# Kernel optimization log

Hardware: AMD Instinct MI355X
Metric: run time of the kernel (lower is better)

Reference implementation:

```python
import jax, jax.numpy as jnp
import numpy as np

B, T, H, N = 4, 512, 32, 64
D = H * N  # n_embd = 2048


def setup_inputs() -> dict:
    key = jax.random.key(0)
    ks = jax.random.split(key, 8)
    f = lambda kk: jax.random.normal(kk, (B, T, H, N), dtype=jnp.float32)
    r = f(ks[0])
    w = f(ks[1])
    k = f(ks[2])
    v = f(ks[3])
    iclr = f(ks[4])
    # int8-style quantized output projection: int values in [-128,127] + per-row scale
    w_out_q = jax.random.randint(ks[5], (D, D), -128, 128, dtype=jnp.int32)
    w_out_scale = jax.random.uniform(ks[6], (D,), dtype=jnp.float32) * 0.01
    return {"r": r, "w": w, "k": k, "v": v, "iclr": iclr,
            "w_out_q": w_out_q, "w_out_scale": w_out_scale}


def _wkv7(r, w, k, v, iclr):
    """RWKV x070 WKV scan. All inputs [B,T,H,N]; returns [B,T,H*N]."""
    decay = jnp.exp(-jnp.exp(w))  # per-channel decay in (0,1), x070 parameterization
    # kk = l2-normalized key direction; a = -kk (removal), b = kk * sigmoid(iclr) (write)
    kk = k * jax.lax.rsqrt(jnp.sum(k * k, axis=-1, keepdims=True) + 1e-12)
    a = -kk
    b = kk * jax.nn.sigmoid(iclr)

    def step(state, inp):
        # state: [B,H,N,N]; each inp element: [B,H,N]
        r_t, d_t, k_t, v_t, a_t, b_t = inp
        sa = jnp.einsum('bhij,bhj->bhi', state, a_t)
        state = (state * d_t[:, :, None, :]
                 + sa[..., None] * b_t[:, :, None, :]
                 + v_t[..., None] * k_t[:, :, None, :])
        y_t = jnp.einsum('bhij,bhj->bhi', state, r_t)
        return state, y_t

    tb = lambda x: jnp.swapaxes(x, 0, 1)  # [B,T,H,N] -> [T,B,H,N]
    state0 = jnp.zeros((B, H, N, N), dtype=r.dtype)
    _, y = jax.lax.scan(step, state0, (tb(r), tb(decay), tb(k), tb(v), tb(a), tb(b)))
    return jnp.swapaxes(y, 0, 1).reshape(B, T, H * N)


def reference(r, w, k, v, iclr, w_out_q, w_out_scale):
    y = _wkv7(r, w, k, v, iclr)               # [B,T,D]
    # inline dequant of quantized output projection (per-output-row scale)
    W = w_out_q.astype(jnp.float32) * w_out_scale[:, None]  # [D,D]
    return jnp.einsum('btd,od->bto', y, W)    # [B,T,D]
```

## Files before the change

### kernel.cpp

```cpp
#include <hip/hip_runtime.h>
#include <hip/hip_bf16.h>
#include <stdint.h>

#define B_ 4
#define T_ 512
#define H_ 32
#define N_ 64
#define D_ 2048
#define M_ (B_*T_)

typedef __attribute__((ext_vector_type(4))) float f32x4;
typedef __attribute__((ext_vector_type(8))) short short8;

template <int CTRL>
__device__ __forceinline__ float dpp_add(float x) {
    int t = __builtin_amdgcn_mov_dpp(__float_as_int(x), CTRL, 0xF, 0xF, true);
    return x + __int_as_float(t);
}
__device__ __forceinline__ float bfly16(float x) {
    x = dpp_add<0xB1>(x);
    x = dpp_add<0x4E>(x);
    x = dpp_add<0x141>(x);
    x = dpp_add<0x140>(x);
    return x;
}

__device__ __forceinline__ void gld16(const float* g, float* l) {
    __builtin_amdgcn_global_load_lds(
        (const __attribute__((address_space(1))) unsigned int*)g,
        (__attribute__((address_space(3))) unsigned int*)l, 16, 0, 0);
}

__global__ __launch_bounds__(256) void prep(
    const float* __restrict__ r, const float* __restrict__ w,
    const float* __restrict__ k, const float* __restrict__ v,
    const float* __restrict__ iclr, const int* __restrict__ q,
    float* __restrict__ pk, __hip_bfloat16* __restrict__ o) {
    if (blockIdx.x >= 16384) {
        int i = ((blockIdx.x - 16384) * 256 + threadIdx.x) * 4;
        int4 qi = *(const int4*)(q + i);
        __hip_bfloat16 t[4];
        t[0] = __float2bfloat16((float)qi.x);
        t[1] = __float2bfloat16((float)qi.y);
        t[2] = __float2bfloat16((float)qi.z);
        t[3] = __float2bfloat16((float)qi.w);
        *(uint2*)(o + i) = *(uint2*)t;
        return;
    }
    int g = blockIdx.x * 4 + (threadIdx.x >> 6);
    int lane = threadIdx.x & 63;
    int b = g >> 14;
    int t = (g >> 5) & (T_ - 1);
    int h = g & 31;
    size_t si = (size_t)g * 64 + lane;
    size_t di = (((size_t)(b * H_ + h) * T_) + t) * 384 + lane;
    float rv = r[si], wv = w[si], kv = k[si], vv = v[si], av = iclr[si];
    float d = expf(-expf(wv));
    float ss = kv * kv;
#pragma unroll
    for (int m = 1; m < 64; m <<= 1) ss += __shfl_xor(ss, m, 64);
    float kkv = kv * rsqrtf(ss + 1e-12f);
    float bbv = kkv * (1.f / (1.f + expf(-av)));
    pk[di          ] = rv;
    pk[di + 1 * 64 ] = kv;
    pk[di + 2 * 64 ] = vv;
    pk[di + 3 * 64 ] = d;
    pk[di + 4 * 64 ] = kkv;
    pk[di + 5 * 64 ] = bbv;
}

__global__ __launch_bounds__(64, 2) void wkv_scan(
    const float* __restrict__ pk, __hip_bfloat16* __restrict__ y) {
    const int bh = blockIdx.x & 127;
    const int wv = blockIdx.x >> 7;
    const int b = bh >> 5, h = bh & 31;
    const int lane = threadIdx.x;
    const int jg = lane & 15;
    const int rl = lane >> 4;
    const int row = wv * 4 + rl;

    __shared__ __align__(16) float ring[2 * 1536];

    const float* src = pk + (size_t)bh * T_ * 384;

#pragma unroll
    for (int gg = 0; gg < 2; ++gg) {
        const float* g0 = src + (size_t)gg * 1536 + lane * 4;
        float* l0 = &ring[gg * 1536];
#pragma unroll
        for (int c = 0; c < 6; ++c)
            gld16(g0 + c * 256, l0 + c * 256);
    }

    float S[4] = {0.f, 0.f, 0.f, 0.f};

    for (int g = 0; g < T_ / 4; ++g) {
        const int slot = g & 1;
        if (g == 0) { asm volatile("s_waitcnt vmcnt(6)"  ::: "memory"); }
        else        { asm volatile("s_waitcnt vmcnt(10)" ::: "memory"); }
        const float* rb0 = &ring[slot * 1536];

#pragma unroll
        for (int i = 0; i < 4; ++i) {
            const int t = g * 4 + i;
            const float* rb = rb0 + i * 384;

            f32x4 Rc = *(const f32x4*)(rb + 0 * 64 + jg * 4);
            f32x4 Kc = *(const f32x4*)(rb + 1 * 64 + jg * 4);
            float vcv =                 rb[2 * 64 + row];
            f32x4 Dc = *(const f32x4*)(rb + 3 * 64 + jg * 4);
            f32x4 Ac = *(const f32x4*)(rb + 4 * 64 + jg * 4);
            f32x4 Bc = *(const f32x4*)(rb + 5 * 64 + jg * 4);

            float s01 = fmaf(S[1], Ac[1], S[0] * Ac[0]);
            float s23 = fmaf(S[3], Ac[3], S[2] * Ac[2]);
            const float sa = -bfly16(s01 + s23);

            float t0 = fmaf(sa, Bc[0], vcv * Kc[0]);
            S[0] = fmaf(S[0], Dc[0], t0);
            float t1 = fmaf(sa, Bc[1], vcv * Kc[1]);
            S[1] = fmaf(S[1], Dc[1], t1);
            float y01 = fmaf(S[1], Rc[1], S[0] * Rc[0]);
            float t2 = fmaf(sa, Bc[2], vcv * Kc[2]);
            S[2] = fmaf(S[2], Dc[2], t2);
            float t3 = fmaf(sa, Bc[3], vcv * Kc[3]);
            S[3] = fmaf(S[3], Dc[3], t3);
            float y23 = fmaf(S[3], Rc[3], S[2] * Rc[2]);
            float ys = bfly16(y01 + y23);
            if (jg == 0)
                y[((size_t)b * T_ + t) * D_ + h * 64 + row] = __float2bfloat16(ys);
        }

        asm volatile("" ::: "memory");
        int gp = g + 2; if (gp > T_ / 4 - 1) gp = T_ / 4 - 1;
        const float* g0 = src + (size_t)gp * 1536 + lane * 4;
        float* l0 = &ring[slot * 1536];
#pragma unroll
        for (int c = 0; c < 6; ++c)
            gld16(g0 + c * 256, l0 + c * 256);
    }
}

__device__ __forceinline__ void gload_lds16(const __hip_bfloat16* g, ushort* l) {
    __builtin_amdgcn_global_load_lds(
        (const __attribute__((address_space(1))) unsigned int*)g,
        (__attribute__((address_space(3))) unsigned int*)l, 16, 0, 0);
}

__global__ __launch_bounds__(256, 1) void gemm_bt(
    const __hip_bfloat16* __restrict__ A,
    const __hip_bfloat16* __restrict__ Bq,
    const float* __restrict__ scale,
    float* __restrict__ C) {
    const int K = D_;
    __shared__ __align__(16) ushort As[128 * 64];
    __shared__ __align__(16) ushort Bs[128 * 64];

    const int tid = threadIdx.x;
    const int lane = tid & 63;
    const int wave = tid >> 6;
    const int wr = wave >> 1, wc = wave & 1;
    const int m0 = blockIdx.x * 128;
    const int n0 = blockIdx.y * 128;

    const int srow8 = lane >> 3;
    const int scol8 = (lane & 7) * 8;
    const int ml = lane & 15;
    const int kq = (lane >> 4) * 8;

    f32x4 acc[4][4] = {};

    for (int k0 = 0; k0 < K; k0 += 64) {
#pragma unroll
        for (int c = 0; c < 4; ++c) {
            int rbase = wave * 32 + c * 8;
            int row = rbase + srow8;
            gload_lds16(A  + (size_t)(m0 + row) * K + k0 + scol8, &As[rbase * 64]);
            gload_lds16(Bq + (size_t)(n0 + row) * K + k0 + scol8, &Bs[rbase * 64]);
        }
        __syncthreads();
#pragma unroll
        for (int ks = 0; ks < 2; ++ks) {
            short8 af[4], bf[4];
#pragma unroll
            for (int tm = 0; tm < 4; ++tm)
                af[tm] = *(const short8*)(&As[(wr * 64 + tm * 16 + ml) * 64 + ks * 32 + kq]);
#pragma unroll
            for (int tn = 0; tn < 4; ++tn)
                bf[tn] = *(const short8*)(&Bs[(wc * 64 + tn * 16 + ml) * 64 + ks * 32 + kq]);
#pragma unroll
            for (int tm = 0; tm < 4; ++tm)
#pragma unroll
                for (int tn = 0; tn < 4; ++tn)
                    acc[tm][tn] = __builtin_amdgcn_mfma_f32_16x16x32_bf16(
                        af[tm], bf[tn], acc[tm][tn], 0, 0, 0);
        }
        __syncthreads();
    }

#pragma unroll
    for (int tn = 0; tn < 4; ++tn) {
        int gn = n0 + wc * 64 + tn * 16 + ml;
        float sc = scale[gn];
#pragma unroll
        for (int tm = 0; tm < 4; ++tm) {
            int gm = m0 + wr * 64 + tm * 16 + (lane >> 4) * 4;
#pragma unroll
            for (int rg = 0; rg < 4; ++rg)
                C[(size_t)(gm + rg) * D_ + gn] = acc[tm][tn][rg] * sc;
        }
    }
}

extern "C" void kernel_launch(void* const* d_in, const int* in_sizes, int n_in,
                              void* d_out, int out_size, void* d_ws, size_t ws_size,
                              hipStream_t stream) {
    (void)in_sizes; (void)n_in; (void)out_size; (void)ws_size;
    const float* r  = (const float*)d_in[0];
    const float* w  = (const float*)d_in[1];
    const float* k  = (const float*)d_in[2];
    const float* v  = (const float*)d_in[3];
    const float* ic = (const float*)d_in[4];
    const int*   wq = (const int*)d_in[5];
    const float* sc = (const float*)d_in[6];
    float* out = (float*)d_out;

    char* p = (char*)d_ws;
    __hip_bfloat16* yb = (__hip_bfloat16*)p;  p += (size_t)M_ * D_ * 2;
    __hip_bfloat16* wb = (__hip_bfloat16*)p;  p += (size_t)D_ * D_ * 2;
    float* pk = (float*)p;

    prep    <<<dim3(16384 + 4096), dim3(256), 0, stream>>>(r, w, k, v, ic, wq, pk, wb);
    wkv_scan<<<dim3(B_ * H_ * 16), dim3(64), 0, stream>>>(pk, yb);
    gemm_bt <<<dim3(M_ / 128, D_ / 128), dim3(256), 0, stream>>>(yb, wb, sc, out);
}
```

Baseline: 298.4 us.

## Overlap weight conversion with scan, prefetch scan operands, shrink GEMM N tile

The int32-to-bf16 weight conversion moves out of the prep kernel and into extra blocks of the scan kernel, so it runs on CUs that the scan's 2048 single-wave blocks leave idle. The scan loop now software-pipelines its LDS operand loads, reading the next timestep's fragment while computing the current one, with an adjusted vmcnt wait. The GEMM tile shrinks from 128x128 to 128x64 with two blocks per CU, doubling the grid to raise occupancy. The risks are more register pressure in the scan, lower data reuse per GEMM tile, and conversion blocks competing with scan blocks for CUs.

```diff
diff --git a/kernel.cpp b/kernel.cpp
--- a/kernel.cpp
+++ b/kernel.cpp
@@ -34,19 +34,7 @@
 __global__ __launch_bounds__(256) void prep(
     const float* __restrict__ r, const float* __restrict__ w,
     const float* __restrict__ k, const float* __restrict__ v,
-    const float* __restrict__ iclr, const int* __restrict__ q,
-    float* __restrict__ pk, __hip_bfloat16* __restrict__ o) {
-    if (blockIdx.x >= 16384) {
-        int i = ((blockIdx.x - 16384) * 256 + threadIdx.x) * 4;
-        int4 qi = *(const int4*)(q + i);
-        __hip_bfloat16 t[4];
-        t[0] = __float2bfloat16((float)qi.x);
-        t[1] = __float2bfloat16((float)qi.y);
-        t[2] = __float2bfloat16((float)qi.z);
-        t[3] = __float2bfloat16((float)qi.w);
-        *(uint2*)(o + i) = *(uint2*)t;
-        return;
-    }
+    const float* __restrict__ iclr, float* __restrict__ pk) {
     int g = blockIdx.x * 4 + (threadIdx.x >> 6);
     int lane = threadIdx.x & 63;
     int b = g >> 14;
@@ -69,8 +57,36 @@
     pk[di + 5 * 64 ] = bbv;
 }
 
+struct Frag {
+    f32x4 R, Kk, Dd, Aa, Bb;
+    float v;
+};
+
+__device__ __forceinline__ Frag ldfrag(const float* rb, int jg, int row) {
+    Frag f;
+    f.R  = *(const f32x4*)(rb + 0 * 64 + jg * 4);
+    f.Kk = *(const f32x4*)(rb + 1 * 64 + jg * 4);
+    f.v  = rb[2 * 64 + row];
+    f.Dd = *(const f32x4*)(rb + 3 * 64 + jg * 4);
+    f.Aa = *(const f32x4*)(rb + 4 * 64 + jg * 4);
+    f.Bb = *(const f32x4*)(rb + 5 * 64 + jg * 4);
+    return f;
+}
+
 __global__ __launch_bounds__(64, 2) void wkv_scan(
-    const float* __restrict__ pk, __hip_bfloat16* __restrict__ y) {
+    const float* __restrict__ pk, __hip_bfloat16* __restrict__ y,
+    const int* __restrict__ q, __hip_bfloat16* __restrict__ o) {
+    if (blockIdx.x >= 2048) {
+        int i = ((blockIdx.x - 2048) * 64 + (int)threadIdx.x) * 4;
+        int4 qi = *(const int4*)(q + i);
+        __hip_bfloat16 t[4];
+        t[0] = __float2bfloat16((float)qi.x);
+        t[1] = __float2bfloat16((float)qi.y);
+        t[2] = __float2bfloat16((float)qi.z);
+        t[3] = __float2bfloat16((float)qi.w);
+        *(uint2*)(o + i) = *(uint2*)t;
+        return;
+    }
     const int bh = blockIdx.x & 127;
     const int wv = blockIdx.x >> 7;
     const int b = bh >> 5, h = bh & 31;
@@ -92,49 +108,48 @@
             gld16(g0 + c * 256, l0 + c * 256);
     }
 
+    asm volatile("s_waitcnt vmcnt(6)" ::: "memory");
+    Frag cur = ldfrag(&ring[0], jg, row);
     float S[4] = {0.f, 0.f, 0.f, 0.f};
 
     for (int g = 0; g < T_ / 4; ++g) {
-        const int slot = g & 1;
-        if (g == 0) { asm volatile("s_waitcnt vmcnt(6)"  ::: "memory"); }
-        else        { asm volatile("s_waitcnt vmcnt(10)" ::: "memory"); }
-        const float* rb0 = &ring[slot * 1536];
-
+        const float* rb0 = &ring[(g & 1) * 1536];
+        const float* nb0 = &ring[((g + 1) & 1) * 1536];
 #pragma unroll
         for (int i = 0; i < 4; ++i) {
-            const int t = g * 4 + i;
-            const float* rb = rb0 + i * 384;
-
-            f32x4 Rc = *(const f32x4*)(rb + 0 * 64 + jg * 4);
-            f32x4 Kc = *(const f32x4*)(rb + 1 * 64 + jg * 4);
-            float vcv =                 rb[2 * 64 + row];
-            f32x4 Dc = *(const f32x4*)(rb + 3 * 64 + jg * 4);
-            f32x4 Ac = *(const f32x4*)(rb + 4 * 64 + jg * 4);
-            f32x4 Bc = *(const f32x4*)(rb + 5 * 64 + jg * 4);
-
-            float s01 = fmaf(S[1], Ac[1], S[0] * Ac[0]);
-            float s23 = fmaf(S[3], Ac[3], S[2] * Ac[2]);
+            Frag nxt;
+            if (i < 3) {
+                nxt = ldfrag(rb0 + (i + 1) * 384, jg, row);
+            } else {
+                asm volatile("s_waitcnt vmcnt(3)" ::: "memory");
+                nxt = ldfrag(nb0, jg, row);
+            }
+
+            float s01 = fmaf(S[1], cur.Aa[1], S[0] * cur.Aa[0]);
+            float s23 = fmaf(S[3], cur.Aa[3], S[2] * cur.Aa[2]);
             const float sa = -bfly16(s01 + s23);
 
-            float t0 = fmaf(sa, Bc[0], vcv * Kc[0]);
-            S[0] = fmaf(S[0], Dc[0], t0);
-            float t1 = fmaf(sa, Bc[1], vcv * Kc[1]);
-            S[1] = fmaf(S[1], Dc[1], t1);
-            float y01 = fmaf(S[1], Rc[1], S[0] * Rc[0]);
-            float t2 = fmaf(sa, Bc[2], vcv * Kc[2]);
-            S[2] = fmaf(S[2], Dc[2], t2);
-            float t3 = fmaf(sa, Bc[3], vcv * Kc[3]);
-            S[3] = fmaf(S[3], Dc[3], t3);
-            float y23 = fmaf(S[3], Rc[3], S[2] * Rc[2]);
+            float t0 = fmaf(sa, cur.Bb[0], cur.v * cur.Kk[0]);
+            S[0] = fmaf(S[0], cur.Dd[0], t0);
+            float t1 = fmaf(sa, cur.Bb[1], cur.v * cur.Kk[1]);
+            S[1] = fmaf(S[1], cur.Dd[1], t1);
+            float y01 = fmaf(S[1], cur.R[1], S[0] * cur.R[0]);
+            float t2 = fmaf(sa, cur.Bb[2], cur.v * cur.Kk[2]);
+            S[2] = fmaf(S[2], cur.Dd[2], t2);
+            float t3 = fmaf(sa, cur.Bb[3], cur.v * cur.Kk[3]);
+            S[3] = fmaf(S[3], cur.Dd[3], t3);
+            float y23 = fmaf(S[3], cur.R[3], S[2] * cur.R[2]);
             float ys = bfly16(y01 + y23);
             if (jg == 0)
-                y[((size_t)b * T_ + t) * D_ + h * 64 + row] = __float2bfloat16(ys);
+                y[((size_t)b * T_ + (g * 4 + i)) * D_ + h * 64 + row] =
+                    __float2bfloat16(ys);
+            cur = nxt;
         }
 
         asm volatile("" ::: "memory");
         int gp = g + 2; if (gp > T_ / 4 - 1) gp = T_ / 4 - 1;
         const float* g0 = src + (size_t)gp * 1536 + lane * 4;
-        float* l0 = &ring[slot * 1536];
+        float* l0 = &ring[(g & 1) * 1536];
 #pragma unroll
         for (int c = 0; c < 6; ++c)
             gld16(g0 + c * 256, l0 + c * 256);
@@ -147,51 +162,56 @@
         (__attribute__((address_space(3))) unsigned int*)l, 16, 0, 0);
 }
 
-__global__ __launch_bounds__(256, 1) void gemm_bt(
+__global__ __launch_bounds__(256, 2) void gemm_bt(
     const __hip_bfloat16* __restrict__ A,
     const __hip_bfloat16* __restrict__ Bq,
     const float* __restrict__ scale,
     float* __restrict__ C) {
     const int K = D_;
     __shared__ __align__(16) ushort As[128 * 64];
-    __shared__ __align__(16) ushort Bs[128 * 64];
+    __shared__ __align__(16) ushort Bs[64 * 64];
 
     const int tid = threadIdx.x;
     const int lane = tid & 63;
     const int wave = tid >> 6;
     const int wr = wave >> 1, wc = wave & 1;
     const int m0 = blockIdx.x * 128;
-    const int n0 = blockIdx.y * 128;
+    const int n0 = blockIdx.y * 64;
 
     const int srow8 = lane >> 3;
     const int scol8 = (lane & 7) * 8;
     const int ml = lane & 15;
     const int kq = (lane >> 4) * 8;
 
-    f32x4 acc[4][4] = {};
+    f32x4 acc[4][2] = {};
 
     for (int k0 = 0; k0 < K; k0 += 64) {
 #pragma unroll
         for (int c = 0; c < 4; ++c) {
-            int rbase = wave * 32 + c * 8;
-            int row = rbase + srow8;
-            gload_lds16(A  + (size_t)(m0 + row) * K + k0 + scol8, &As[rbase * 64]);
-            gload_lds16(Bq + (size_t)(n0 + row) * K + k0 + scol8, &Bs[rbase * 64]);
+            int ra = wave * 32 + c * 8;
+            gload_lds16(A + (size_t)(m0 + ra + srow8) * K + k0 + scol8,
+                        &As[ra * 64]);
+        }
+#pragma unroll
+        for (int c = 0; c < 2; ++c) {
+            int rb = wave * 16 + c * 8;
+            gload_lds16(Bq + (size_t)(n0 + rb + srow8) * K + k0 + scol8,
+                        &Bs[rb * 64]);
         }
         __syncthreads();
 #pragma unroll
         for (int ks = 0; ks < 2; ++ks) {
-            short8 af[4], bf[4];
+            short8 af[4], bf[2];
 #pragma unroll
             for (int tm = 0; tm < 4; ++tm)
                 af[tm] = *(const short8*)(&As[(wr * 64 + tm * 16 + ml) * 64 + ks * 32 + kq]);
 #pragma unroll
-            for (int tn = 0; tn < 4; ++tn)
-                bf[tn] = *(const short8*)(&Bs[(wc * 64 + tn * 16 + ml) * 64 + ks * 32 + kq]);
+            for (int tn = 0; tn < 2; ++tn)
+                bf[tn] = *(const short8*)(&Bs[(wc * 32 + tn * 16 + ml) * 64 + ks * 32 + kq]);
 #pragma unroll
             for (int tm = 0; tm < 4; ++tm)
 #pragma unroll
-                for (int tn = 0; tn < 4; ++tn)
+                for (int tn = 0; tn < 2; ++tn)
                     acc[tm][tn] = __builtin_amdgcn_mfma_f32_16x16x32_bf16(
                         af[tm], bf[tn], acc[tm][tn], 0, 0, 0);
         }
@@ -199,8 +219,8 @@
     }
 
 #pragma unroll
-    for (int tn = 0; tn < 4; ++tn) {
-        int gn = n0 + wc * 64 + tn * 16 + ml;
+    for (int tn = 0; tn < 2; ++tn) {
+        int gn = n0 + wc * 32 + tn * 16 + ml;
         float sc = scale[gn];
 #pragma unroll
         for (int tm = 0; tm < 4; ++tm) {
@@ -230,7 +250,7 @@
     __hip_bfloat16* wb = (__hip_bfloat16*)p;  p += (size_t)D_ * D_ * 2;
     float* pk = (float*)p;
 
-    prep    <<<dim3(16384 + 4096), dim3(256), 0, stream>>>(r, w, k, v, ic, wq, pk, wb);
-    wkv_scan<<<dim3(B_ * H_ * 16), dim3(64), 0, stream>>>(pk, yb);
-    gemm_bt <<<dim3(M_ / 128, D_ / 128), dim3(256), 0, stream>>>(yb, wb, sc, out);
-}
+    prep    <<<dim3(16384), dim3(256), 0, stream>>>(r, w, k, v, ic, pk);
+    wkv_scan<<<dim3(2048 + 16384), dim3(64), 0, stream>>>(pk, yb, wq, wb);
+    gemm_bt <<<dim3(M_ / 128, D_ / 64), dim3(256), 0, stream>>>(yb, wb, sc, out);
+}
```

Measured after the change: 282.9 us. 5.2% less time.

## Merge scan waves into shared-ring blocks, overlap weight cast, double-buffer GEMM

Applied to the files above, without the earlier changes.

The scan now uses 512-thread blocks, each covering half the rows of one head. A single wave streams the shared input ring and barriers synchronise the other waves, so the 8x redundant per-wave global loads go away. The int-to-bf16 weight conversion moves from prep into extra blocks of the scan launch, so it can fill the otherwise idle GPU during the sequential scan. The GEMM switches to 128x64 tiles with double-buffered LDS staging, a swizzled block order and two blocks per CU. The costs are added barrier overhead inside the latency-bound scan loop and smaller GEMM tiles.

```diff
diff --git a/kernel.cpp b/kernel.cpp
--- a/kernel.cpp
+++ b/kernel.cpp
@@ -34,19 +34,7 @@
 __global__ __launch_bounds__(256) void prep(
     const float* __restrict__ r, const float* __restrict__ w,
     const float* __restrict__ k, const float* __restrict__ v,
-    const float* __restrict__ iclr, const int* __restrict__ q,
-    float* __restrict__ pk, __hip_bfloat16* __restrict__ o) {
-    if (blockIdx.x >= 16384) {
-        int i = ((blockIdx.x - 16384) * 256 + threadIdx.x) * 4;
-        int4 qi = *(const int4*)(q + i);
-        __hip_bfloat16 t[4];
-        t[0] = __float2bfloat16((float)qi.x);
-        t[1] = __float2bfloat16((float)qi.y);
-        t[2] = __float2bfloat16((float)qi.z);
-        t[3] = __float2bfloat16((float)qi.w);
-        *(uint2*)(o + i) = *(uint2*)t;
-        return;
-    }
+    const float* __restrict__ iclr, float* __restrict__ pk) {
     int g = blockIdx.x * 4 + (threadIdx.x >> 6);
     int lane = threadIdx.x & 63;
     int b = g >> 14;
@@ -69,36 +57,52 @@
     pk[di + 5 * 64 ] = bbv;
 }
 
-__global__ __launch_bounds__(64, 2) void wkv_scan(
-    const float* __restrict__ pk, __hip_bfloat16* __restrict__ y) {
-    const int bh = blockIdx.x & 127;
-    const int wv = blockIdx.x >> 7;
+__global__ __launch_bounds__(512) void wkv_scan(
+    const float* __restrict__ pk, __hip_bfloat16* __restrict__ y,
+    const int* __restrict__ q, __hip_bfloat16* __restrict__ o) {
+    if (blockIdx.x >= 256) {
+        int i = ((blockIdx.x - 256) * 512 + (int)threadIdx.x) * 4;
+        int4 qi = *(const int4*)(q + i);
+        __hip_bfloat16 t[4];
+        t[0] = __float2bfloat16((float)qi.x);
+        t[1] = __float2bfloat16((float)qi.y);
+        t[2] = __float2bfloat16((float)qi.z);
+        t[3] = __float2bfloat16((float)qi.w);
+        *(uint2*)(o + i) = *(uint2*)t;
+        return;
+    }
+    const int bh   = blockIdx.x & 127;
+    const int half = blockIdx.x >> 7;
+    const int tid  = threadIdx.x;
+    const int wave = tid >> 6;
+    const int lane = tid & 63;
     const int b = bh >> 5, h = bh & 31;
-    const int lane = threadIdx.x;
     const int jg = lane & 15;
     const int rl = lane >> 4;
-    const int row = wv * 4 + rl;
+    const int row = (half * 8 + wave) * 4 + rl;
 
     __shared__ __align__(16) float ring[2 * 1536];
 
     const float* src = pk + (size_t)bh * T_ * 384;
 
-#pragma unroll
-    for (int gg = 0; gg < 2; ++gg) {
-        const float* g0 = src + (size_t)gg * 1536 + lane * 4;
-        float* l0 = &ring[gg * 1536];
-#pragma unroll
-        for (int c = 0; c < 6; ++c)
-            gld16(g0 + c * 256, l0 + c * 256);
+    if (wave == 0) {
+#pragma unroll
+        for (int gg = 0; gg < 2; ++gg)
+#pragma unroll
+            for (int c = 0; c < 6; ++c)
+                gld16(src + gg * 1536 + c * 256 + lane * 4,
+                      &ring[gg * 1536 + c * 256]);
     }
 
     float S[4] = {0.f, 0.f, 0.f, 0.f};
 
     for (int g = 0; g < T_ / 4; ++g) {
-        const int slot = g & 1;
-        if (g == 0) { asm volatile("s_waitcnt vmcnt(6)"  ::: "memory"); }
-        else        { asm volatile("s_waitcnt vmcnt(10)" ::: "memory"); }
-        const float* rb0 = &ring[slot * 1536];
+        if (wave == 0) {
+            if (g == 0) { asm volatile("s_waitcnt vmcnt(6)"  ::: "memory"); }
+            else        { asm volatile("s_waitcnt vmcnt(10)" ::: "memory"); }
+        }
+        asm volatile("s_barrier" ::: "memory");
+        const float* rb0 = &ring[(g & 1) * 1536];
 
 #pragma unroll
         for (int i = 0; i < 4; ++i) {
@@ -131,13 +135,16 @@
                 y[((size_t)b * T_ + t) * D_ + h * 64 + row] = __float2bfloat16(ys);
         }
 
-        asm volatile("" ::: "memory");
-        int gp = g + 2; if (gp > T_ / 4 - 1) gp = T_ / 4 - 1;
-        const float* g0 = src + (size_t)gp * 1536 + lane * 4;
-        float* l0 = &ring[slot * 1536];
-#pragma unroll
-        for (int c = 0; c < 6; ++c)
-            gld16(g0 + c * 256, l0 + c * 256);
+        asm volatile("s_barrier" ::: "memory");
+
+        if (wave == 0) {
+            int gp = g + 2; if (gp > T_ / 4 - 1) gp = T_ / 4 - 1;
+            const float* g0 = src + (size_t)gp * 1536 + lane * 4;
+            float* l0 = &ring[(g & 1) * 1536];
+#pragma unroll
+            for (int c = 0; c < 6; ++c)
+                gld16(g0 + c * 256, l0 + c * 256);
+        }
     }
 }
 
@@ -147,60 +154,82 @@
         (__attribute__((address_space(3))) unsigned int*)l, 16, 0, 0);
 }
 
-__global__ __launch_bounds__(256, 1) void gemm_bt(
+__global__ __launch_bounds__(256, 2) void gemm_bt(
     const __hip_bfloat16* __restrict__ A,
     const __hip_bfloat16* __restrict__ Bq,
     const float* __restrict__ scale,
     float* __restrict__ C) {
     const int K = D_;
-    __shared__ __align__(16) ushort As[128 * 64];
-    __shared__ __align__(16) ushort Bs[128 * 64];
+    __shared__ __align__(16) ushort As[2][128 * 64];
+    __shared__ __align__(16) ushort Bs[2][64 * 64];
 
     const int tid = threadIdx.x;
     const int lane = tid & 63;
     const int wave = tid >> 6;
     const int wr = wave >> 1, wc = wave & 1;
-    const int m0 = blockIdx.x * 128;
-    const int n0 = blockIdx.y * 128;
+
+    const int id = blockIdx.x;
+    const int swz = (id & 7) * 64 + (id >> 3);
+    const int m0 = (swz & 15) * 128;
+    const int n0 = (swz >> 4) * 64;
 
     const int srow8 = lane >> 3;
     const int scol8 = (lane & 7) * 8;
     const int ml = lane & 15;
     const int kq = (lane >> 4) * 8;
 
-    f32x4 acc[4][4] = {};
-
-    for (int k0 = 0; k0 < K; k0 += 64) {
-#pragma unroll
-        for (int c = 0; c < 4; ++c) {
-            int rbase = wave * 32 + c * 8;
-            int row = rbase + srow8;
-            gload_lds16(A  + (size_t)(m0 + row) * K + k0 + scol8, &As[rbase * 64]);
-            gload_lds16(Bq + (size_t)(n0 + row) * K + k0 + scol8, &Bs[rbase * 64]);
-        }
-        __syncthreads();
+    f32x4 acc[4][2] = {};
+
+#define GSTAGE(slot, kk0)                                                    \
+    {                                                                        \
+        _Pragma("unroll")                                                    \
+        for (int c = 0; c < 4; ++c) {                                        \
+            int ra = wave * 32 + c * 8;                                      \
+            gload_lds16(A + (size_t)(m0 + ra + srow8) * K + (kk0) + scol8,   \
+                        &As[slot][ra * 64]);                                 \
+        }                                                                    \
+        _Pragma("unroll")                                                    \
+        for (int c = 0; c < 2; ++c) {                                        \
+            int rb = wave * 16 + c * 8;                                      \
+            gload_lds16(Bq + (size_t)(n0 + rb + srow8) * K + (kk0) + scol8,  \
+                        &Bs[slot][rb * 64]);                                 \
+        }                                                                    \
+    }
+
+    GSTAGE(0, 0);
+
+    for (int t = 0; t < K / 64; ++t) {
+        if (t + 1 < K / 64) {
+            GSTAGE((t + 1) & 1, (t + 1) * 64);
+            asm volatile("s_waitcnt vmcnt(6)" ::: "memory");
+        } else {
+            asm volatile("s_waitcnt vmcnt(0)" ::: "memory");
+        }
+        asm volatile("s_barrier" ::: "memory");
+        const int sl = t & 1;
 #pragma unroll
         for (int ks = 0; ks < 2; ++ks) {
-            short8 af[4], bf[4];
+            short8 af[4], bf[2];
 #pragma unroll
             for (int tm = 0; tm < 4; ++tm)
-                af[tm] = *(const short8*)(&As[(wr * 64 + tm * 16 + ml) * 64 + ks * 32 + kq]);
-#pragma unroll
-            for (int tn = 0; tn < 4; ++tn)
-                bf[tn] = *(const short8*)(&Bs[(wc * 64 + tn * 16 + ml) * 64 + ks * 32 + kq]);
+                af[tm] = *(const short8*)(&As[sl][(wr * 64 + tm * 16 + ml) * 64 + ks * 32 + kq]);
+#pragma unroll
+            for (int tn = 0; tn < 2; ++tn)
+                bf[tn] = *(const short8*)(&Bs[sl][(wc * 32 + tn * 16 + ml) * 64 + ks * 32 + kq]);
 #pragma unroll
             for (int tm = 0; tm < 4; ++tm)
 #pragma unroll
-                for (int tn = 0; tn < 4; ++tn)
+                for (int tn = 0; tn < 2; ++tn)
                     acc[tm][tn] = __builtin_amdgcn_mfma_f32_16x16x32_bf16(
                         af[tm], bf[tn], acc[tm][tn], 0, 0, 0);
         }
-        __syncthreads();
-    }
-
-#pragma unroll
-    for (int tn = 0; tn < 4; ++tn) {
-        int gn = n0 + wc * 64 + tn * 16 + ml;
+        asm volatile("s_barrier" ::: "memory");
+    }
+#undef GSTAGE
+
+#pragma unroll
+    for (int tn = 0; tn < 2; ++tn) {
+        int gn = n0 + wc * 32 + tn * 16 + ml;
         float sc = scale[gn];
 #pragma unroll
         for (int tm = 0; tm < 4; ++tm) {
@@ -230,7 +259,7 @@
     __hip_bfloat16* wb = (__hip_bfloat16*)p;  p += (size_t)D_ * D_ * 2;
     float* pk = (float*)p;
 
-    prep    <<<dim3(16384 + 4096), dim3(256), 0, stream>>>(r, w, k, v, ic, wq, pk, wb);
-    wkv_scan<<<dim3(B_ * H_ * 16), dim3(64), 0, stream>>>(pk, yb);
-    gemm_bt <<<dim3(M_ / 128, D_ / 128), dim3(256), 0, stream>>>(yb, wb, sc, out);
-}
+    prep    <<<dim3(16384), dim3(256), 0, stream>>>(r, w, k, v, ic, pk);
+    wkv_scan<<<dim3(256 + 2048), dim3(512), 0, stream>>>(pk, yb, wq, wb);
+    gemm_bt <<<dim3(512), dim3(256), 0, stream>>>(yb, wb, sc, out);
+}
```

Result: faster. 287.8 us (-3.6%).
